# Kernel optimization log

Measured on AMD Instinct MI355X. Metric: run time of the kernel, lower is better.

## Reference

```python
import jax, jax.numpy as jnp
import numpy as np

NUM_INSTANCES = 8
NUM_HEADS = 4
EPS = 1e-12  # F.normalize eps


def _l2norm(t):
    # F.normalize(t, dim=-1): t / max(||t||_2, eps) along last axis
    n = jnp.sqrt(jnp.sum(t * t, axis=-1, keepdims=True))
    return t / jnp.maximum(n, EPS)


def setup_inputs() -> dict:
    key = jax.random.key(0)
    ks = jax.random.split(key, 10)
    B, C, H, W = 8, 256, 32, 32
    I = NUM_INSTANCES
    s = 0.05
    return {
        "x": jax.random.normal(ks[0], (B, C, H, W), dtype=jnp.float32),
        "w_inst": jax.random.normal(ks[1], (I, C), dtype=jnp.float32) * s,
        "b_inst": jnp.zeros((I,), dtype=jnp.float32),
        "w_q": jax.random.normal(ks[2], (C, C), dtype=jnp.float32) * s,
        "b_q": jnp.zeros((C,), dtype=jnp.float32),
        "w_k": jax.random.normal(ks[3], (C, C), dtype=jnp.float32) * s,
        "b_k": jnp.zeros((C,), dtype=jnp.float32),
        "w_v": jax.random.normal(ks[4], (C, C), dtype=jnp.float32) * s,
        "b_v": jnp.zeros((C,), dtype=jnp.float32),
    }


def reference(x, w_inst, b_inst, w_q, b_q, w_k, b_k, w_v, b_v):
    B, C, H, W = x.shape
    HW = H * W
    hd = C // NUM_HEADS
    scale = 1.0 / jnp.sqrt(jnp.float32(hd))

    # instance_conv (1x1) + softmax over instance axis
    inst = jnp.einsum('ic,bchw->bihw', w_inst, x) + b_inst[None, :, None, None]
    inst = jax.nn.softmax(inst, axis=1)          # [B, I, H, W]
    masks = jnp.transpose(inst, (1, 0, 2, 3))    # [I, B, H, W] for scan

    def step(acc, mask):                          # mask: [B, H, W]
        feat = (x * mask[:, None]).reshape(B, C, HW)  # masked features
        q = (jnp.einsum('oc,bcn->bon', w_q, feat) + b_q[:, None]).reshape(B, NUM_HEADS, hd, HW)
        k = (jnp.einsum('oc,bcn->bon', w_k, feat) + b_k[:, None]).reshape(B, NUM_HEADS, hd, HW)
        v = (jnp.einsum('oc,bcn->bon', w_v, feat) + b_v[:, None]).reshape(B, NUM_HEADS, hd, HW)
        q = _l2norm(q)
        k = _l2norm(k)
        scores = jnp.einsum('bhci,bhcj->bhij', q, k) * scale  # [B,h,HW,HW]
        attn = jax.nn.softmax(scores, axis=-1)
        att = jnp.einsum('bhij,bhcj->bhci', attn, v).reshape(B, C, H, W)
        return acc + att * mask[:, None], None

    out, _ = jax.lax.scan(step, jnp.zeros_like(x), masks)
    return out
```

## Files before the change

### kernel.cpp

```cpp
#include <hip/hip_runtime.h>
#include <hip/hip_fp16.h>

#define NB 8
#define NC 256
#define NHW 1024
#define NI 8
#define NH 4
#define HD 64
#define EPS 1e-12f
#define QSC  64.0f
#define QSCI 0.015625f

typedef _Float16 f16;
typedef __attribute__((ext_vector_type(8))) _Float16 half8;
typedef __attribute__((ext_vector_type(4))) float floatx4;

union H8 { half8 h8; __half2 h2[4]; uint4 u4; f16 e[8]; };
union H4 { uint2 u2; __half2 h2[2]; f16 e[4]; };

__global__ __launch_bounds__(256) void k_mask_part(
    const float* __restrict__ x, const float* __restrict__ w_inst,
    float* __restrict__ part_m, f16* __restrict__ xt)
{
    __shared__ float w_s[NI][32];
    __shared__ __align__(16) f16 xls[32][264];
    int nt = blockIdx.x, b = blockIdx.y, cc = blockIdx.z;
    int tid = threadIdx.x;
    w_s[tid >> 5][tid & 31] = w_inst[(tid >> 5)*NC + cc*32 + (tid & 31)];
    __syncthreads();
    int n = nt*256 + tid;
    const float* xp = x + ((size_t)(b*NC + cc*32))*NHW + n;
    float acc[NI] = {};
    for (int c = 0; c < 32; ++c) {
        float xv = xp[(size_t)c*NHW];
        xls[c][tid] = (f16)xv;
#pragma unroll
        for (int i = 0; i < NI; ++i) acc[i] = fmaf(w_s[i][c], xv, acc[i]);
    }
#pragma unroll
    for (int i = 0; i < NI; ++i)
        part_m[((size_t)(cc*NI + i)*NB + b)*NHW + n] = acc[i];
    __syncthreads();
#pragma unroll
    for (int it = 0; it < 4; ++it) {
        int r = (tid >> 2) + it*64;
        int c8 = (tid & 3)*8;
        H8 v;
#pragma unroll
        for (int i = 0; i < 8; ++i) v.e[i] = xls[c8 + i][r];
        *(uint4*)(xt + ((size_t)(b*NHW + nt*256 + r))*NC + cc*32 + c8) = v.u4;
    }
}

__global__ __launch_bounds__(256) void k_mask_comb(
    const float* __restrict__ part_m, const float* __restrict__ b_inst,
    float* __restrict__ masks)
{
    int nt = blockIdx.x, b = blockIdx.y;
    int n = nt*256 + threadIdx.x;
    float a[NI];
#pragma unroll
    for (int i = 0; i < NI; ++i) {
        float s = b_inst[i];
#pragma unroll
        for (int cc = 0; cc < 8; ++cc)
            s += part_m[((size_t)(cc*NI + i)*NB + b)*NHW + n];
        a[i] = s;
    }
    float m = a[0];
#pragma unroll
    for (int i = 1; i < NI; ++i) m = fmaxf(m, a[i]);
    float ssum = 0.f;
#pragma unroll
    for (int i = 0; i < NI; ++i) { a[i] = __expf(a[i]-m); ssum += a[i]; }
    float inv = 1.0f/ssum;
#pragma unroll
    for (int i = 0; i < NI; ++i) masks[((size_t)i*NB + b)*NHW + n] = a[i]*inv;
}

__global__ __launch_bounds__(256) void k_wcast(
    const float* __restrict__ wq, const float* __restrict__ wk, const float* __restrict__ wv,
    f16* __restrict__ w16)
{
    int m = blockIdx.y;
    const float* src = (m == 0) ? wq : (m == 1) ? wk : wv;
    int e0 = (blockIdx.x*256 + threadIdx.x)*8;
    float4 a = *(const float4*)(src + e0);
    float4 c = *(const float4*)(src + e0 + 4);
    H8 h;
    h.h2[0] = __floats2half2_rn(a.x, a.y);
    h.h2[1] = __floats2half2_rn(a.z, a.w);
    h.h2[2] = __floats2half2_rn(c.x, c.y);
    h.h2[3] = __floats2half2_rn(c.z, c.w);
    *(uint4*)(w16 + (size_t)m*NC*NC + e0) = h.u4;
}

__global__ __launch_bounds__(256) void k_gemm_mfma(
    const f16* __restrict__ xt, const f16* __restrict__ w16,
    f16* __restrict__ Gqt, f16* __restrict__ Gkt, f16* __restrict__ Gv)
{
    __shared__ __align__(16) char glds[30720];
    int tid = threadIdx.x;
    int nt = blockIdx.x, ot = blockIdx.y;
    int m = blockIdx.z >> 3, b = blockIdx.z & 7;
    int o0 = ot*64;
    int w = tid >> 6, lane = tid & 63, quad = lane >> 4, l15 = lane & 15;
    const f16* wm = w16 + (size_t)m*NC*NC;
    const f16* xb = xt + (size_t)b*NHW*NC + (size_t)nt*128*NC;
    f16* wt0 = (f16*)glds;
    f16* xt0 = (f16*)(glds + 10240);
    int srow = tid >> 2, scol = (tid & 3)*8;

    floatx4 acc[2][4];
#pragma unroll
    for (int nm=0;nm<2;nm++)
#pragma unroll
        for (int om=0;om<4;om++){ acc[nm][om][0]=0.f; acc[nm][om][1]=0.f;
                                  acc[nm][om][2]=0.f; acc[nm][om][3]=0.f; }
    *(uint4*)&wt0[(0*64 + srow)*40 + scol]      = *(const uint4*)(wm + (size_t)(o0+srow)*NC + scol);
    *(uint4*)&xt0[(0*128 + srow)*40 + scol]     = *(const uint4*)(xb + (size_t)srow*NC + scol);
    *(uint4*)&xt0[(0*128 + 64+srow)*40 + scol]  = *(const uint4*)(xb + (size_t)(64+srow)*NC + scol);

    for (int k = 0; k < 8; ++k) {
        int p = k & 1;
        __syncthreads();
        if (k < 7) {
            int q = 1 - p, kc = (k+1)*32;
            *(uint4*)&wt0[(q*64 + srow)*40 + scol]     = *(const uint4*)(wm + (size_t)(o0+srow)*NC + kc + scol);
            *(uint4*)&xt0[(q*128 + srow)*40 + scol]    = *(const uint4*)(xb + (size_t)srow*NC + kc + scol);
            *(uint4*)&xt0[(q*128 + 64+srow)*40 + scol] = *(const uint4*)(xb + (size_t)(64+srow)*NC + kc + scol);
        }
        H8 wa[4], xa[2];
#pragma unroll
        for (int om = 0; om < 4; ++om)
            wa[om].u4 = *(const uint4*)&wt0[(p*64 + om*16 + l15)*40 + quad*8];
#pragma unroll
        for (int nm = 0; nm < 2; ++nm)
            xa[nm].u4 = *(const uint4*)&xt0[(p*128 + w*32 + nm*16 + l15)*40 + quad*8];
#pragma unroll
        for (int nm = 0; nm < 2; ++nm)
#pragma unroll
            for (int om = 0; om < 4; ++om)
                acc[nm][om] = __builtin_amdgcn_mfma_f32_16x16x32_f16(wa[om].h8, xa[nm].h8, acc[nm][om], 0, 0, 0);
    }
    __syncthreads();
    if (m < 2) {
        f16* lt = (f16*)glds;
#pragma unroll
        for (int nm = 0; nm < 2; ++nm)
#pragma unroll
            for (int om = 0; om < 4; ++om) {
                H4 pk;
#pragma unroll
                for (int r = 0; r < 4; ++r) pk.e[r] = (f16)acc[nm][om][r];
                *(uint2*)&lt[(size_t)(w*32 + nm*16 + l15)*72 + om*16 + quad*4] = pk.u2;
            }
        __syncthreads();
        f16* dst = (m == 0) ? Gqt : Gkt;
#pragma unroll
        for (int it = 0; it < 4; ++it) {
            int row = (tid >> 3) + it*32;
            int c8 = (tid & 7)*8;
            uint4 v = *(const uint4*)&lt[(size_t)row*72 + c8];
            *(uint4*)(dst + ((size_t)(b*NHW + nt*128 + row))*NC + o0 + c8) = v;
        }
    } else {
        f16* lv = (f16*)glds;
#pragma unroll
        for (int nm = 0; nm < 2; ++nm)
#pragma unroll
            for (int om = 0; om < 4; ++om)
#pragma unroll
                for (int r = 0; r < 4; ++r)
                    lv[(size_t)(om*16 + quad*4 + r)*136 + w*32 + nm*16 + l15] = (f16)acc[nm][om][r];
        __syncthreads();
#pragma unroll
        for (int it = 0; it < 4; ++it) {
            int row = (tid >> 4) + it*16;
            int n8 = (tid & 15)*8;
            uint4 v = *(const uint4*)&lv[(size_t)row*136 + n8];
            *(uint4*)(Gv + ((size_t)(b*NC + o0 + row))*NHW + nt*128 + n8) = v;
        }
    }
}

__global__ __launch_bounds__(256) void k_norm_part(
    const f16* __restrict__ Gqt, const f16* __restrict__ Gkt,
    const float* __restrict__ masks,
    const float* __restrict__ bq, const float* __restrict__ bk,
    float* __restrict__ part_nq, float* __restrict__ part_nk)
{
    __shared__ float m_s[NI][32];
    int nc = blockIdx.x, b = blockIdx.y;
    int c = threadIdx.x;
    int n0 = nc*32;
    m_s[c >> 5][c & 31] = masks[((size_t)(c >> 5)*NB + b)*NHW + n0 + (c & 31)];
    __syncthreads();
    float bqv = bq[c], bkv = bk[c];
    const f16* gq = Gqt + ((size_t)b*NHW + n0)*NC + c;
    const f16* gk = Gkt + ((size_t)b*NHW + n0)*NC + c;
    float aq[NI] = {}, ak[NI] = {};
    for (int t = 0; t < 32; ++t) {
        float g1 = (float)gq[(size_t)t*NC];
        float g2 = (float)gk[(size_t)t*NC];
#pragma unroll
        for (int i = 0; i < NI; ++i) {
            float mm = m_s[i][t];
            float e = fmaf(mm, g1, bqv); aq[i] = fmaf(e, e, aq[i]);
            e = fmaf(mm, g2, bkv);       ak[i] = fmaf(e, e, ak[i]);
        }
    }
#pragma unroll
    for (int i = 0; i < NI; ++i) {
        part_nq[((size_t)(nc*NI + i)*NB + b)*NC + c] = aq[i];
        part_nk[((size_t)(nc*NI + i)*NB + b)*NC + c] = ak[i];
    }
}

__global__ __launch_bounds__(256) void k_norm_fin(
    const float* __restrict__ part_nq, const float* __restrict__ part_nk,
    float* __restrict__ scale_q, float* __restrict__ scale_k)
{
    int b = blockIdx.x, i = blockIdx.y, c = threadIdx.x;
    float sq = 0.f, sk = 0.f;
#pragma unroll
    for (int nc = 0; nc < 32; ++nc) {
        sq += part_nq[((size_t)(nc*NI + i)*NB + b)*NC + c];
        sk += part_nk[((size_t)(nc*NI + i)*NB + b)*NC + c];
    }
    scale_q[((size_t)i*NB + b)*NC + c] = 0.125f / fmaxf(sqrtf(sq), EPS);
    scale_k[((size_t)i*NB + b)*NC + c] = 1.0f   / fmaxf(sqrtf(sk), EPS);
}

__global__ __launch_bounds__(256,2) void k_attn6(
    const f16* __restrict__ Gqt, const f16* __restrict__ Gkt, const f16* __restrict__ Gv,
    const float* __restrict__ masks,
    const float* __restrict__ bq, const float* __restrict__ bv,
    const float* __restrict__ scale_q, const float* __restrict__ scale_k,
    float* __restrict__ out)
{
    __shared__ __align__(16) f16 kh_s[64][72];
    __shared__ __align__(16) f16 vh_s[64][72];
    __shared__ __align__(16) f16 ph_s[4][32][72];
    __shared__ __align__(16) float mi_s[NI][64];

    int tid = threadIdx.x, bid = blockIdx.x;
    int b = bid & 7, qt = (bid >> 3) & 31, h = bid >> 8;
    int qt0 = qt*32, c0 = h*HD;
    int w = tid >> 6, lane = tid & 63, quad = lane >> 4, l15 = lane & 15;
    int i0 = 2*w;
    f16* ph = &ph_s[w][0][0];

    H8 graw[2][2];
    const f16* gqp = Gqt + ((size_t)b*NHW + qt0)*NC + c0;
#pragma unroll
    for (int qi = 0; qi < 2; ++qi)
#pragma unroll
        for (int ks = 0; ks < 2; ++ks)
            graw[qi][ks].u4 = *(const uint4*)(gqp + (size_t)(qi*16 + l15)*NC + ks*32 + quad*8);

    float mqf[2][2];
#pragma unroll
    for (int ii = 0; ii < 2; ++ii)
#pragma unroll
        for (int qi = 0; qi < 2; ++qi)
            mqf[ii][qi] = masks[((size_t)(i0+ii)*NB + b)*NHW + qt0 + qi*16 + l15];

    H8 qa[2][2][2];
#pragma unroll
    for (int ks = 0; ks < 2; ++ks) {
        int cb = c0 + ks*32 + quad*8;
        float4 bq0 = *(const float4*)(bq + cb);
        float4 bq1 = *(const float4*)(bq + cb + 4);
#pragma unroll
        for (int ii = 0; ii < 2; ++ii) {
            int inst = i0 + ii;
            const float* sqg = scale_q + ((size_t)inst*NB + b)*NC;
            const float* skg = scale_k + ((size_t)inst*NB + b)*NC;
            float4 s0 = *(const float4*)(sqg + cb);
            float4 s1 = *(const float4*)(sqg + cb + 4);
            float4 t0 = *(const float4*)(skg + cb);
            float4 t1 = *(const float4*)(skg + cb + 4);
            float ss[8] = {s0.x*t0.x*QSC, s0.y*t0.y*QSC, s0.z*t0.z*QSC, s0.w*t0.w*QSC,
                           s1.x*t1.x*QSC, s1.y*t1.y*QSC, s1.z*t1.z*QSC, s1.w*t1.w*QSC};
            float bb[8] = {bq0.x*ss[0], bq0.y*ss[1], bq0.z*ss[2], bq0.w*ss[3],
                           bq1.x*ss[4], bq1.y*ss[5], bq1.z*ss[6], bq1.w*ss[7]};
            __half2 sh[4], bh[4];
#pragma unroll
            for (int t = 0; t < 4; ++t) {
                sh[t] = __floats2half2_rn(ss[2*t], ss[2*t+1]);
                bh[t] = __floats2half2_rn(bb[2*t], bb[2*t+1]);
            }
#pragma unroll
            for (int qi = 0; qi < 2; ++qi) {
                __half2 mq2 = __float2half2_rn(mqf[ii][qi]);
#pragma unroll
                for (int t = 0; t < 4; ++t)
                    qa[ii][qi][ks].h2[t] = __hfma2(mq2, __hmul2(graw[qi][ks].h2[t], sh[t]), bh[t]);
            }
        }
    }

    floatx4 acc[2][4][2];
#pragma unroll
    for (int ii=0;ii<2;ii++)
#pragma unroll
        for (int cm=0;cm<4;cm++)
#pragma unroll
            for (int qi=0;qi<2;qi++) { acc[ii][cm][qi][0]=0.f; acc[ii][cm][qi][1]=0.f;
                                       acc[ii][cm][qi][2]=0.f; acc[ii][cm][qi][3]=0.f; }
    float l[2][2] = {};

    for (int j0 = 0; j0 < NHW; j0 += 64) {
        __syncthreads();
#pragma unroll
        for (int t = 0; t < 2; ++t) {
            int chk = tid + t*256;
            int jr = chk >> 3, cc = chk & 7;
            *(uint4*)&kh_s[jr][cc*8] = *(const uint4*)(Gkt + ((size_t)b*NHW + j0 + jr)*NC + c0 + cc*8);
            *(uint4*)&vh_s[jr][cc*8] = *(const uint4*)(Gv + ((size_t)b*NC + c0 + jr)*NHW + j0 + cc*8);
        }
        {
            int i = tid >> 5, jj = (tid & 31)*2;
            *(float2*)&mi_s[i][jj] = *(const float2*)(masks + ((size_t)i*NB + b)*NHW + j0 + jj);
        }
        __syncthreads();
        H8 ka[4][2], va[4][2];
#pragma unroll
        for (int jm = 0; jm < 4; ++jm)
#pragma unroll
            for (int ks = 0; ks < 2; ++ks) {
                ka[jm][ks].u4 = *(const uint4*)&kh_s[jm*16 + l15][ks*32 + quad*8];
                va[jm][ks].u4 = *(const uint4*)&vh_s[jm*16 + l15][ks*32 + quad*8];
            }
#pragma unroll
        for (int ii = 0; ii < 2; ++ii) {
            int inst = i0 + ii;
#pragma unroll
            for (int jm = 0; jm < 4; ++jm) {
                floatx4 s0 = {0.f,0.f,0.f,0.f}, s1 = {0.f,0.f,0.f,0.f};
#pragma unroll
                for (int ks = 0; ks < 2; ++ks) {
                    s0 = __builtin_amdgcn_mfma_f32_16x16x32_f16(ka[jm][ks].h8, qa[ii][0][ks].h8, s0, 0, 0, 0);
                    s1 = __builtin_amdgcn_mfma_f32_16x16x32_f16(ka[jm][ks].h8, qa[ii][1][ks].h8, s1, 0, 0, 0);
                }
                float4 mj4 = *(const float4*)&mi_s[inst][jm*16 + quad*4];
                float mj[4] = {mj4.x, mj4.y, mj4.z, mj4.w};
                float p0[4], p1[4];
#pragma unroll
                for (int r = 0; r < 4; ++r) {
                    float e0 = __expf(s0[r]*(mj[r]*QSCI)); l[ii][0] += e0; p0[r] = e0*mj[r];
                    float e1 = __expf(s1[r]*(mj[r]*QSCI)); l[ii][1] += e1; p1[r] = e1*mj[r];
                }
                H4 pk0, pk1;
                pk0.h2[0] = __floats2half2_rn(p0[0], p0[1]);
                pk0.h2[1] = __floats2half2_rn(p0[2], p0[3]);
                pk1.h2[0] = __floats2half2_rn(p1[0], p1[1]);
                pk1.h2[1] = __floats2half2_rn(p1[2], p1[3]);
                *(uint2*)&ph[(size_t)l15*72      + jm*16 + quad*4] = pk0.u2;
                *(uint2*)&ph[(size_t)(16+l15)*72 + jm*16 + quad*4] = pk1.u2;
            }
            H8 pb[2][2];
#pragma unroll
            for (int qi = 0; qi < 2; ++qi)
#pragma unroll
                for (int ks = 0; ks < 2; ++ks)
                    pb[qi][ks].u4 = *(const uint4*)&ph[(size_t)(qi*16 + l15)*72 + ks*32 + quad*8];
#pragma unroll
            for (int cm = 0; cm < 4; ++cm)
#pragma unroll
                for (int ks = 0; ks < 2; ++ks) {
                    acc[ii][cm][0] = __builtin_amdgcn_mfma_f32_16x16x32_f16(va[cm][ks].h8, pb[0][ks].h8, acc[ii][cm][0], 0, 0, 0);
                    acc[ii][cm][1] = __builtin_amdgcn_mfma_f32_16x16x32_f16(va[cm][ks].h8, pb[1][ks].h8, acc[ii][cm][1], 0, 0, 0);
                }
        }
    }

    float f[2][2];
#pragma unroll
    for (int ii = 0; ii < 2; ++ii)
#pragma unroll
        for (int qi = 0; qi < 2; ++qi) {
            float lv = l[ii][qi];
            lv += __shfl_xor(lv, 16, 64);
            lv += __shfl_xor(lv, 32, 64);
            f[ii][qi] = mqf[ii][qi] / lv;
        }
    float* bufA = (float*)&ph_s[0][0][0];
    float* bufB = bufA + 2304;
    __syncthreads();
    if (w < 2) {
        float* rb = w ? bufB : bufA;
#pragma unroll
        for (int cm = 0; cm < 4; ++cm)
#pragma unroll
            for (int qi = 0; qi < 2; ++qi)
#pragma unroll
                for (int r = 0; r < 4; ++r)
                    rb[(cm*16 + quad*4 + r)*36 + qi*16 + l15] =
                        f[0][qi]*acc[0][cm][qi][r] + f[1][qi]*acc[1][cm][qi][r];
    }
    __syncthreads();
    if (w >= 2) {
        float* rb = (w == 3) ? bufB : bufA;
#pragma unroll
        for (int cm = 0; cm < 4; ++cm)
#pragma unroll
            for (int qi = 0; qi < 2; ++qi)
#pragma unroll
                for (int r = 0; r < 4; ++r)
                    rb[(cm*16 + quad*4 + r)*36 + qi*16 + l15] +=
                        f[0][qi]*acc[0][cm][qi][r] + f[1][qi]*acc[1][cm][qi][r];
    }
    __syncthreads();
    int cc2 = tid >> 2, qg = (tid & 3)*8;
    float bvv = bv[c0 + cc2];
    float* op = out + ((size_t)(b*NC + c0 + cc2))*NHW + qt0;
#pragma unroll
    for (int t = 0; t < 2; ++t) {
        float4 va4 = *(const float4*)&bufA[cc2*36 + qg + t*4];
        float4 vb4 = *(const float4*)&bufB[cc2*36 + qg + t*4];
        float4 v;
        v.x = va4.x + vb4.x + bvv; v.y = va4.y + vb4.y + bvv;
        v.z = va4.z + vb4.z + bvv; v.w = va4.w + vb4.w + bvv;
        *(float4*)(op + qg + t*4) = v;
    }
}

extern "C" void kernel_launch(void* const* d_in, const int* in_sizes, int n_in,
                              void* d_out, int out_size, void* d_ws, size_t ws_size,
                              hipStream_t stream)
{
    const float* x      = (const float*)d_in[0];
    const float* w_inst = (const float*)d_in[1];
    const float* b_inst = (const float*)d_in[2];
    const float* wq = (const float*)d_in[3];
    const float* bq = (const float*)d_in[4];
    const float* wk = (const float*)d_in[5];
    const float* bk = (const float*)d_in[6];
    const float* wv = (const float*)d_in[7];
    const float* bv = (const float*)d_in[8];
    float* out = (float*)d_out;

    float* masks   = (float*)d_ws;
    float* scale_q = masks + (size_t)NI*NB*NHW;
    float* scale_k = scale_q + (size_t)NI*NB*NC;
    f16*   Gqt     = (f16*)(scale_k + (size_t)NI*NB*NC);
    f16*   Gkt     = Gqt + (size_t)NB*NHW*NC;
    f16*   Gv      = Gkt + (size_t)NB*NHW*NC;
    f16*   xt      = Gv + (size_t)NB*NC*NHW;
    f16*   w16     = xt + (size_t)NB*NHW*NC;
    float* part_m  = (float*)(w16 + (size_t)3*NC*NC);
    float* part_nq = part_m + (size_t)8*NI*NB*NHW;
    float* part_nk = part_nq + (size_t)32*NI*NB*NC;

    k_mask_part<<<dim3(4, NB, 8), 256, 0, stream>>>(x, w_inst, part_m, xt);
    k_wcast<<<dim3(32, 3), 256, 0, stream>>>(wq, wk, wv, w16);
    k_mask_comb<<<dim3(4, NB), 256, 0, stream>>>(part_m, b_inst, masks);
    k_gemm_mfma<<<dim3(8, 4, 24), 256, 0, stream>>>(xt, w16, Gqt, Gkt, Gv);
    k_norm_part<<<dim3(32, NB), 256, 0, stream>>>(Gqt, Gkt, masks, bq, bk, part_nq, part_nk);
    k_norm_fin<<<dim3(NB, NI), 256, 0, stream>>>(part_nq, part_nk, scale_q, scale_k);
    k_attn6<<<dim3(1024), 256, 0, stream>>>(Gqt, Gkt, Gv, masks, bq, bv,
                                            scale_q, scale_k, out);
}
```

Measured before the change: 241.0 us.

## Fuse weight cast and mask softmax into neighbours; double-buffer attention with async LDS loads

The separate weight-cast kernel is removed, and the GEMM now converts fp32 weights to fp16 as it loads them. The mask softmax kernel is folded into the norm kernel, cutting two launches. The attention kernel moves to 32-key tiles that are double-buffered in LDS through global_load_lds, with XOR-swizzled layouts. This lets the next tile's K/V/mask loads overlap the MFMA work and leaves one barrier per tile. The trade-offs are the GEMM re-converting weights in every block and the attention loop running twice as many smaller iterations.

```diff
diff --git a/kernel.cpp b/kernel.cpp
--- a/kernel.cpp
+++ b/kernel.cpp
@@ -18,6 +18,12 @@
 union H8 { half8 h8; __half2 h2[4]; uint4 u4; f16 e[8]; };
 union H4 { uint2 u2; __half2 h2[2]; f16 e[4]; };
 
+__device__ __forceinline__ void gll16(const void* g, void* l) {
+    __builtin_amdgcn_global_load_lds(
+        (const __attribute__((address_space(1))) unsigned int*)g,
+        (__attribute__((address_space(3))) unsigned int*)l, 16, 0, 0);
+}
+
 __global__ __launch_bounds__(256) void k_mask_part(
     const float* __restrict__ x, const float* __restrict__ w_inst,
     float* __restrict__ part_m, f16* __restrict__ xt)
@@ -52,60 +58,18 @@
     }
 }
 
-__global__ __launch_bounds__(256) void k_mask_comb(
-    const float* __restrict__ part_m, const float* __restrict__ b_inst,
-    float* __restrict__ masks)
-{
-    int nt = blockIdx.x, b = blockIdx.y;
-    int n = nt*256 + threadIdx.x;
-    float a[NI];
-#pragma unroll
-    for (int i = 0; i < NI; ++i) {
-        float s = b_inst[i];
-#pragma unroll
-        for (int cc = 0; cc < 8; ++cc)
-            s += part_m[((size_t)(cc*NI + i)*NB + b)*NHW + n];
-        a[i] = s;
-    }
-    float m = a[0];
-#pragma unroll
-    for (int i = 1; i < NI; ++i) m = fmaxf(m, a[i]);
-    float ssum = 0.f;
-#pragma unroll
-    for (int i = 0; i < NI; ++i) { a[i] = __expf(a[i]-m); ssum += a[i]; }
-    float inv = 1.0f/ssum;
-#pragma unroll
-    for (int i = 0; i < NI; ++i) masks[((size_t)i*NB + b)*NHW + n] = a[i]*inv;
-}
-
-__global__ __launch_bounds__(256) void k_wcast(
+__global__ __launch_bounds__(256) void k_gemm_mfma(
+    const f16* __restrict__ xt,
     const float* __restrict__ wq, const float* __restrict__ wk, const float* __restrict__ wv,
-    f16* __restrict__ w16)
-{
-    int m = blockIdx.y;
-    const float* src = (m == 0) ? wq : (m == 1) ? wk : wv;
-    int e0 = (blockIdx.x*256 + threadIdx.x)*8;
-    float4 a = *(const float4*)(src + e0);
-    float4 c = *(const float4*)(src + e0 + 4);
-    H8 h;
-    h.h2[0] = __floats2half2_rn(a.x, a.y);
-    h.h2[1] = __floats2half2_rn(a.z, a.w);
-    h.h2[2] = __floats2half2_rn(c.x, c.y);
-    h.h2[3] = __floats2half2_rn(c.z, c.w);
-    *(uint4*)(w16 + (size_t)m*NC*NC + e0) = h.u4;
-}
-
-__global__ __launch_bounds__(256) void k_gemm_mfma(
-    const f16* __restrict__ xt, const f16* __restrict__ w16,
     f16* __restrict__ Gqt, f16* __restrict__ Gkt, f16* __restrict__ Gv)
 {
     __shared__ __align__(16) char glds[30720];
     int tid = threadIdx.x;
     int nt = blockIdx.x, ot = blockIdx.y;
     int m = blockIdx.z >> 3, b = blockIdx.z & 7;
+    const float* wsel = (m == 0) ? wq : (m == 1) ? wk : wv;
     int o0 = ot*64;
     int w = tid >> 6, lane = tid & 63, quad = lane >> 4, l15 = lane & 15;
-    const f16* wm = w16 + (size_t)m*NC*NC;
     const f16* xb = xt + (size_t)b*NHW*NC + (size_t)nt*128*NC;
     f16* wt0 = (f16*)glds;
     f16* xt0 = (f16*)(glds + 10240);
@@ -117,16 +81,27 @@
 #pragma unroll
         for (int om=0;om<4;om++){ acc[nm][om][0]=0.f; acc[nm][om][1]=0.f;
                                   acc[nm][om][2]=0.f; acc[nm][om][3]=0.f; }
-    *(uint4*)&wt0[(0*64 + srow)*40 + scol]      = *(const uint4*)(wm + (size_t)(o0+srow)*NC + scol);
-    *(uint4*)&xt0[(0*128 + srow)*40 + scol]     = *(const uint4*)(xb + (size_t)srow*NC + scol);
-    *(uint4*)&xt0[(0*128 + 64+srow)*40 + scol]  = *(const uint4*)(xb + (size_t)(64+srow)*NC + scol);
-
+    {
+        float4 a4 = *(const float4*)(wsel + (size_t)(o0+srow)*NC + scol);
+        float4 b4 = *(const float4*)(wsel + (size_t)(o0+srow)*NC + scol + 4);
+        H8 hw;
+        hw.h2[0] = __floats2half2_rn(a4.x, a4.y); hw.h2[1] = __floats2half2_rn(a4.z, a4.w);
+        hw.h2[2] = __floats2half2_rn(b4.x, b4.y); hw.h2[3] = __floats2half2_rn(b4.z, b4.w);
+        *(uint4*)&wt0[(0*64 + srow)*40 + scol] = hw.u4;
+        *(uint4*)&xt0[(0*128 + srow)*40 + scol]    = *(const uint4*)(xb + (size_t)srow*NC + scol);
+        *(uint4*)&xt0[(0*128 + 64+srow)*40 + scol] = *(const uint4*)(xb + (size_t)(64+srow)*NC + scol);
+    }
     for (int k = 0; k < 8; ++k) {
         int p = k & 1;
         __syncthreads();
         if (k < 7) {
             int q = 1 - p, kc = (k+1)*32;
-            *(uint4*)&wt0[(q*64 + srow)*40 + scol]     = *(const uint4*)(wm + (size_t)(o0+srow)*NC + kc + scol);
+            float4 a4 = *(const float4*)(wsel + (size_t)(o0+srow)*NC + kc + scol);
+            float4 b4 = *(const float4*)(wsel + (size_t)(o0+srow)*NC + kc + scol + 4);
+            H8 hw;
+            hw.h2[0] = __floats2half2_rn(a4.x, a4.y); hw.h2[1] = __floats2half2_rn(a4.z, a4.w);
+            hw.h2[2] = __floats2half2_rn(b4.x, b4.y); hw.h2[3] = __floats2half2_rn(b4.z, b4.w);
+            *(uint4*)&wt0[(q*64 + srow)*40 + scol] = hw.u4;
             *(uint4*)&xt0[(q*128 + srow)*40 + scol]    = *(const uint4*)(xb + (size_t)srow*NC + kc + scol);
             *(uint4*)&xt0[(q*128 + 64+srow)*40 + scol] = *(const uint4*)(xb + (size_t)(64+srow)*NC + kc + scol);
         }
@@ -184,18 +159,40 @@
     }
 }
 
-__global__ __launch_bounds__(256) void k_norm_part(
+__global__ __launch_bounds__(256) void k_norm_mask(
+    const float* __restrict__ part_m, const float* __restrict__ b_inst,
     const f16* __restrict__ Gqt, const f16* __restrict__ Gkt,
-    const float* __restrict__ masks,
     const float* __restrict__ bq, const float* __restrict__ bk,
-    float* __restrict__ part_nq, float* __restrict__ part_nk)
-{
+    float* __restrict__ masks, float* __restrict__ part_nq, float* __restrict__ part_nk)
+{
+    __shared__ float lg[NI][32];
     __shared__ float m_s[NI][32];
     int nc = blockIdx.x, b = blockIdx.y;
-    int c = threadIdx.x;
+    int tid = threadIdx.x;
     int n0 = nc*32;
-    m_s[c >> 5][c & 31] = masks[((size_t)(c >> 5)*NB + b)*NHW + n0 + (c & 31)];
-    __syncthreads();
+    {
+        int nl = tid & 31, i = tid >> 5;
+        float s = b_inst[i];
+#pragma unroll
+        for (int cc = 0; cc < 8; ++cc)
+            s += part_m[((size_t)(cc*NI + i)*NB + b)*NHW + n0 + nl];
+        lg[i][nl] = s;
+    }
+    __syncthreads();
+    {
+        int nl = tid & 31, i = tid >> 5;
+        float mx = lg[0][nl];
+#pragma unroll
+        for (int k = 1; k < NI; ++k) mx = fmaxf(mx, lg[k][nl]);
+        float ssum = 0.f;
+#pragma unroll
+        for (int k = 0; k < NI; ++k) ssum += __expf(lg[k][nl] - mx);
+        float mv = __expf(lg[i][nl] - mx) / ssum;
+        m_s[i][nl] = mv;
+        masks[((size_t)i*NB + b)*NHW + n0 + nl] = mv;
+    }
+    __syncthreads();
+    int c = tid;
     float bqv = bq[c], bkv = bk[c];
     const f16* gq = Gqt + ((size_t)b*NHW + n0)*NC + c;
     const f16* gk = Gkt + ((size_t)b*NHW + n0)*NC + c;
@@ -232,24 +229,24 @@
     scale_k[((size_t)i*NB + b)*NC + c] = 1.0f   / fmaxf(sqrtf(sk), EPS);
 }
 
-__global__ __launch_bounds__(256,2) void k_attn6(
+__global__ __launch_bounds__(256,2) void k_attn7(
     const f16* __restrict__ Gqt, const f16* __restrict__ Gkt, const f16* __restrict__ Gv,
     const float* __restrict__ masks,
     const float* __restrict__ bq, const float* __restrict__ bv,
     const float* __restrict__ scale_q, const float* __restrict__ scale_k,
     float* __restrict__ out)
 {
-    __shared__ __align__(16) f16 kh_s[64][72];
-    __shared__ __align__(16) f16 vh_s[64][72];
-    __shared__ __align__(16) f16 ph_s[4][32][72];
-    __shared__ __align__(16) float mi_s[NI][64];
+    __shared__ __align__(16) char lds[38912];
+    f16*   KH = (f16*)lds;
+    f16*   VH = (f16*)(lds + 8192);
+    float* MI = (float*)(lds + 16384);
+    f16*   PH = (f16*)(lds + 18432);
 
     int tid = threadIdx.x, bid = blockIdx.x;
     int b = bid & 7, qt = (bid >> 3) & 31, h = bid >> 8;
     int qt0 = qt*32, c0 = h*HD;
     int w = tid >> 6, lane = tid & 63, quad = lane >> 4, l15 = lane & 15;
     int i0 = 2*w;
-    f16* ph = &ph_s[w][0][0];
 
     H8 graw[2][2];
     const f16* gqp = Gqt + ((size_t)b*NHW + qt0)*NC + c0;
@@ -258,14 +255,12 @@
 #pragma unroll
         for (int ks = 0; ks < 2; ++ks)
             graw[qi][ks].u4 = *(const uint4*)(gqp + (size_t)(qi*16 + l15)*NC + ks*32 + quad*8);
-
     float mqf[2][2];
 #pragma unroll
     for (int ii = 0; ii < 2; ++ii)
 #pragma unroll
         for (int qi = 0; qi < 2; ++qi)
             mqf[ii][qi] = masks[((size_t)(i0+ii)*NB + b)*NHW + qt0 + qi*16 + l15];
-
     H8 qa[2][2][2];
 #pragma unroll
     for (int ks = 0; ks < 2; ++ks) {
@@ -301,6 +296,12 @@
         }
     }
 
+    int kjr = tid >> 3, kdc = (tid & 7) ^ (kjr & 7);
+    int vcr = tid >> 2, vdc = (tid & 3) ^ (vcr & 3);
+    const f16* kgb = Gkt + (size_t)b*NHW*NC + c0 + kdc*8;
+    const f16* vgb = Gv + ((size_t)(b*NC + c0 + vcr))*NHW + vdc*8;
+    const float* mgb = masks + ((size_t)(lane >> 3)*NB + b)*NHW + (lane & 7)*4;
+
     floatx4 acc[2][4][2];
 #pragma unroll
     for (int ii=0;ii<2;ii++)
@@ -311,40 +312,35 @@
                                        acc[ii][cm][qi][2]=0.f; acc[ii][cm][qi][3]=0.f; }
     float l[2][2] = {};
 
-    for (int j0 = 0; j0 < NHW; j0 += 64) {
-        __syncthreads();
-#pragma unroll
-        for (int t = 0; t < 2; ++t) {
-            int chk = tid + t*256;
-            int jr = chk >> 3, cc = chk & 7;
-            *(uint4*)&kh_s[jr][cc*8] = *(const uint4*)(Gkt + ((size_t)b*NHW + j0 + jr)*NC + c0 + cc*8);
-            *(uint4*)&vh_s[jr][cc*8] = *(const uint4*)(Gv + ((size_t)b*NC + c0 + jr)*NHW + j0 + cc*8);
-        }
-        {
-            int i = tid >> 5, jj = (tid & 31)*2;
-            *(float2*)&mi_s[i][jj] = *(const float2*)(masks + ((size_t)i*NB + b)*NHW + j0 + jj);
-        }
-        __syncthreads();
-        H8 ka[4][2], va[4][2];
-#pragma unroll
-        for (int jm = 0; jm < 4; ++jm)
-#pragma unroll
-            for (int ks = 0; ks < 2; ++ks) {
-                ka[jm][ks].u4 = *(const uint4*)&kh_s[jm*16 + l15][ks*32 + quad*8];
-                va[jm][ks].u4 = *(const uint4*)&vh_s[jm*16 + l15][ks*32 + quad*8];
-            }
-#pragma unroll
-        for (int ii = 0; ii < 2; ++ii) {
-            int inst = i0 + ii;
-#pragma unroll
-            for (int jm = 0; jm < 4; ++jm) {
+    gll16(kgb + (size_t)kjr*NC, KH + tid*8);
+    gll16(vgb, VH + tid*8);
+    if (w == 0) gll16(mgb, MI + lane*4);
+    __syncthreads();
+
+    int p = 0;
+    for (int j0 = 0; j0 < NHW; j0 += 32) {
+        int jn = (j0 + 32) & (NHW - 1);
+        gll16(kgb + (size_t)(jn + kjr)*NC, KH + (p^1)*2048 + tid*8);
+        gll16(vgb + jn, VH + (p^1)*2048 + tid*8);
+        if (w == 0) gll16(mgb + jn, MI + (p^1)*256 + lane*4);
+
+        const f16* kh = KH + p*2048;
+        const f16* vh = VH + p*2048;
+        const float* mi = MI + p*256;
+#pragma unroll
+        for (int jm = 0; jm < 2; ++jm) {
+            int krow = jm*16 + l15;
+            H8 ka0, ka1;
+            ka0.u4 = *(const uint4*)&kh[krow*64 + ((quad       ^ (l15 & 7))*8)];
+            ka1.u4 = *(const uint4*)&kh[krow*64 + (((4 + quad) ^ (l15 & 7))*8)];
+#pragma unroll
+            for (int ii = 0; ii < 2; ++ii) {
                 floatx4 s0 = {0.f,0.f,0.f,0.f}, s1 = {0.f,0.f,0.f,0.f};
-#pragma unroll
-                for (int ks = 0; ks < 2; ++ks) {
-                    s0 = __builtin_amdgcn_mfma_f32_16x16x32_f16(ka[jm][ks].h8, qa[ii][0][ks].h8, s0, 0, 0, 0);
-                    s1 = __builtin_amdgcn_mfma_f32_16x16x32_f16(ka[jm][ks].h8, qa[ii][1][ks].h8, s1, 0, 0, 0);
-                }
-                float4 mj4 = *(const float4*)&mi_s[inst][jm*16 + quad*4];
+                s0 = __builtin_amdgcn_mfma_f32_16x16x32_f16(ka0.h8, qa[ii][0][0].h8, s0, 0, 0, 0);
+                s0 = __builtin_amdgcn_mfma_f32_16x16x32_f16(ka1.h8, qa[ii][0][1].h8, s0, 0, 0, 0);
+                s1 = __builtin_amdgcn_mfma_f32_16x16x32_f16(ka0.h8, qa[ii][1][0].h8, s1, 0, 0, 0);
+                s1 = __builtin_amdgcn_mfma_f32_16x16x32_f16(ka1.h8, qa[ii][1][1].h8, s1, 0, 0, 0);
+                float4 mj4 = *(const float4*)&mi[(i0+ii)*32 + jm*16 + quad*4];
                 float mj[4] = {mj4.x, mj4.y, mj4.z, mj4.w};
                 float p0[4], p1[4];
 #pragma unroll
@@ -357,23 +353,29 @@
                 pk0.h2[1] = __floats2half2_rn(p0[2], p0[3]);
                 pk1.h2[0] = __floats2half2_rn(p1[0], p1[1]);
                 pk1.h2[1] = __floats2half2_rn(p1[2], p1[3]);
-                *(uint2*)&ph[(size_t)l15*72      + jm*16 + quad*4] = pk0.u2;
-                *(uint2*)&ph[(size_t)(16+l15)*72 + jm*16 + quad*4] = pk1.u2;
+                f16* ph = PH + w*2560 + ii*1280;
+                *(uint2*)&ph[l15*40      + jm*16 + quad*4] = pk0.u2;
+                *(uint2*)&ph[(16+l15)*40 + jm*16 + quad*4] = pk1.u2;
             }
-            H8 pb[2][2];
-#pragma unroll
-            for (int qi = 0; qi < 2; ++qi)
-#pragma unroll
-                for (int ks = 0; ks < 2; ++ks)
-                    pb[qi][ks].u4 = *(const uint4*)&ph[(size_t)(qi*16 + l15)*72 + ks*32 + quad*8];
-#pragma unroll
-            for (int cm = 0; cm < 4; ++cm)
-#pragma unroll
-                for (int ks = 0; ks < 2; ++ks) {
-                    acc[ii][cm][0] = __builtin_amdgcn_mfma_f32_16x16x32_f16(va[cm][ks].h8, pb[0][ks].h8, acc[ii][cm][0], 0, 0, 0);
-                    acc[ii][cm][1] = __builtin_amdgcn_mfma_f32_16x16x32_f16(va[cm][ks].h8, pb[1][ks].h8, acc[ii][cm][1], 0, 0, 0);
-                }
-        }
+        }
+        H8 pb[2][2];
+#pragma unroll
+        for (int ii = 0; ii < 2; ++ii) {
+            const f16* ph = PH + w*2560 + ii*1280;
+            pb[ii][0].u4 = *(const uint4*)&ph[l15*40      + quad*8];
+            pb[ii][1].u4 = *(const uint4*)&ph[(16+l15)*40 + quad*8];
+        }
+#pragma unroll
+        for (int cm = 0; cm < 4; ++cm) {
+            H8 va;
+            va.u4 = *(const uint4*)&vh[(cm*16 + l15)*32 + ((quad ^ (l15 & 3))*8)];
+            acc[0][cm][0] = __builtin_amdgcn_mfma_f32_16x16x32_f16(va.h8, pb[0][0].h8, acc[0][cm][0], 0, 0, 0);
+            acc[0][cm][1] = __builtin_amdgcn_mfma_f32_16x16x32_f16(va.h8, pb[0][1].h8, acc[0][cm][1], 0, 0, 0);
+            acc[1][cm][0] = __builtin_amdgcn_mfma_f32_16x16x32_f16(va.h8, pb[1][0].h8, acc[1][cm][0], 0, 0, 0);
+            acc[1][cm][1] = __builtin_amdgcn_mfma_f32_16x16x32_f16(va.h8, pb[1][1].h8, acc[1][cm][1], 0, 0, 0);
+        }
+        __syncthreads();
+        p ^= 1;
     }
 
     float f[2][2];
@@ -386,9 +388,8 @@
             lv += __shfl_xor(lv, 32, 64);
             f[ii][qi] = mqf[ii][qi] / lv;
         }
-    float* bufA = (float*)&ph_s[0][0][0];
+    float* bufA = (float*)lds;
     float* bufB = bufA + 2304;
-    __syncthreads();
     if (w < 2) {
         float* rb = w ? bufB : bufA;
 #pragma unroll
@@ -449,17 +450,15 @@
     f16*   Gkt     = Gqt + (size_t)NB*NHW*NC;
     f16*   Gv      = Gkt + (size_t)NB*NHW*NC;
     f16*   xt      = Gv + (size_t)NB*NC*NHW;
-    f16*   w16     = xt + (size_t)NB*NHW*NC;
-    float* part_m  = (float*)(w16 + (size_t)3*NC*NC);
+    float* part_m  = (float*)(xt + (size_t)NB*NHW*NC);
     float* part_nq = part_m + (size_t)8*NI*NB*NHW;
     float* part_nk = part_nq + (size_t)32*NI*NB*NC;
 
     k_mask_part<<<dim3(4, NB, 8), 256, 0, stream>>>(x, w_inst, part_m, xt);
-    k_wcast<<<dim3(32, 3), 256, 0, stream>>>(wq, wk, wv, w16);
-    k_mask_comb<<<dim3(4, NB), 256, 0, stream>>>(part_m, b_inst, masks);
-    k_gemm_mfma<<<dim3(8, 4, 24), 256, 0, stream>>>(xt, w16, Gqt, Gkt, Gv);
-    k_norm_part<<<dim3(32, NB), 256, 0, stream>>>(Gqt, Gkt, masks, bq, bk, part_nq, part_nk);
+    k_gemm_mfma<<<dim3(8, 4, 24), 256, 0, stream>>>(xt, wq, wk, wv, Gqt, Gkt, Gv);
+    k_norm_mask<<<dim3(32, NB), 256, 0, stream>>>(part_m, b_inst, Gqt, Gkt, bq, bk,
+                                                  masks, part_nq, part_nk);
     k_norm_fin<<<dim3(NB, NI), 256, 0, stream>>>(part_nq, part_nk, scale_q, scale_k);
-    k_attn6<<<dim3(1024), 256, 0, stream>>>(Gqt, Gkt, Gv, masks, bq, bv,
+    k_attn7<<<dim3(1024), 256, 0, stream>>>(Gqt, Gkt, Gv, masks, bq, bv,
                                             scale_q, scale_k, out);
 }
```

Result: faster. 230.1 us (-4.5%).
